# Kernel tuning notes

Hardware: AMD Instinct MI355X
Metric: run time of the kernel (lower is better)

The kernel has to match this reference:

```python
import jax, jax.numpy as jnp
import numpy as np

N_NODES = 50000
N_EDGES = 600000
IN_DIM = 128
OUT_DIM = 128
N_REL = 32
N_BASES = 4
BN_EPS = 1e-5


def setup_inputs() -> dict:
    key = jax.random.key(0)
    ks = jax.random.split(key, 8)
    entity_emb = jax.random.normal(ks[0], (N_NODES, IN_DIM), dtype=jnp.float32)
    bases = jax.random.normal(ks[1], (N_BASES, IN_DIM, OUT_DIM), dtype=jnp.float32) * 0.05
    coefficients = jax.random.normal(ks[2], (N_REL, N_BASES), dtype=jnp.float32) * 0.5
    W_loop = jax.random.normal(ks[3], (IN_DIM, OUT_DIM), dtype=jnp.float32) * 0.05
    b_loop = jnp.zeros((OUT_DIM,), dtype=jnp.float32)
    gamma = jnp.ones((OUT_DIM,), dtype=jnp.float32)
    beta = jnp.zeros((OUT_DIM,), dtype=jnp.float32)
    edge_index = jax.random.randint(ks[4], (2, N_EDGES), 0, N_NODES, dtype=jnp.int32)
    edge_type = jax.random.randint(ks[5], (N_EDGES,), 0, N_REL, dtype=jnp.int32)
    return {"entity_emb": entity_emb, "bases": bases, "coefficients": coefficients,
            "W_loop": W_loop, "b_loop": b_loop, "gamma": gamma, "beta": beta,
            "edge_index": edge_index, "edge_type": edge_type}


def reference(entity_emb, bases, coefficients, W_loop, b_loop, gamma, beta, edge_index, edge_type):
    N = entity_emb.shape[0]
    # self-loop linear
    out = entity_emb @ W_loop + b_loop  # [N, out_dim]
    # basis decomposition: per-relation weight W[r] = sum_b coeff[r,b] * bases[b]
    W = jnp.einsum('rb,bio->rio', coefficients, bases)  # [R, in, out]
    src, dst = edge_index[0], edge_index[1]
    # per-edge message: entity_emb[src_e] @ W[edge_type_e]  (vectorizes the per-relation loop)
    msg = jnp.einsum('ei,eio->eo', entity_emb[src], W[edge_type])  # [E, out]
    out = out + jax.ops.segment_sum(msg, dst, num_segments=N)
    # degree normalization (in-degree over all edges, clamped at 1)
    deg = jax.ops.segment_sum(jnp.ones_like(dst, dtype=out.dtype), dst, num_segments=N)
    out = out / jnp.maximum(deg, 1.0)[:, None]
    # BatchNorm1d (training mode: biased batch stats over node dim)
    mean = jnp.mean(out, axis=0)
    var = jnp.mean((out - mean) ** 2, axis=0)
    out = (out - mean) / jnp.sqrt(var + BN_EPS) * gamma + beta
    return jax.nn.relu(out)
```

## Files before the change

kernel.cpp:

```cpp
#include <hip/hip_runtime.h>
#include <cstdint>

#define NN 50000
#define NE 600000
#define NPAIRS 1563
#define GSTRIDE 512

typedef unsigned short ushort_t;
typedef __bf16 bf16_t;
typedef __attribute__((ext_vector_type(8))) bf16_t bf16x8;
typedef __attribute__((ext_vector_type(8))) ushort_t ushort8;
typedef __attribute__((ext_vector_type(4))) float f32x4;
typedef __attribute__((ext_vector_type(2))) float f32x2;

#define WT_OFF   0ul
#define XG_OFF   40960ul
#define XBF_OFF  16040960ul
#define CNT_OFF  19240960ul
#define CUR_OFF  19290960ul
#define BSUM_OFF 19340960ul
#define BSCN_OFF 19341088ul
#define CS_OFF   19341216ul
#define CSQ_OFF  19341344ul

__device__ __forceinline__ float2 bf2_to_f2(uint32_t u) {
    float2 r;
    r.x = __uint_as_float(u << 16);
    r.y = __uint_as_float(u & 0xffff0000u);
    return r;
}

__device__ __forceinline__ ushort_t f2bf(float f) {
    uint32_t u = __float_as_uint(f);
    u = (u + 0x7fffu + ((u >> 16) & 1u)) >> 16;
    return (ushort_t)u;
}

__device__ __forceinline__ uint32_t f2bf2(float x, float y) {
    return (uint32_t)f2bf(x) | ((uint32_t)f2bf(y) << 16);
}

__device__ __forceinline__ void async_copy16(const void* g, void* l) {
    __builtin_amdgcn_global_load_lds(
        (const __attribute__((address_space(1))) void*)g,
        (__attribute__((address_space(3))) void*)l, 16, 0, 0);
}

__global__ __launch_bounds__(256) void k_prep(
    const float* __restrict__ Wl, const float* __restrict__ bases,
    ushort_t* __restrict__ WT)
{
    const int i = blockIdx.x * 256 + threadIdx.x;
    if (i >= 128 * 640) return;
    const int n = i / 640;
    const int kk = i - n * 640;
    float v;
    if (kk < 128) v = Wl[kk * 128 + n];
    else {
        const int j = kk - 128;
        v = bases[(size_t)(j >> 7) * 16384 + (j & 127) * 128 + n];
    }
    WT[i] = f2bf(v);
}

__global__ __launch_bounds__(256) void k_cast(
    const float* __restrict__ X, ushort_t* __restrict__ Xbf,
    ushort_t* __restrict__ XG)
{
    __shared__ ushort_t L[16][136];
    const int tid = threadIdx.x;
    const int tile = blockIdx.x;
    {
        const int row = tid >> 4, gc = tid & 15;
        const int node = tile * 16 + row;
        const float4* p = (const float4*)(X + (size_t)node * 128 + gc * 8);
        const float4 a = p[0], b = p[1];
        ushort_t t8[8] = { f2bf(a.x), f2bf(a.y), f2bf(a.z), f2bf(a.w),
                           f2bf(b.x), f2bf(b.y), f2bf(b.z), f2bf(b.w) };
        const uint4 v = *(const uint4*)t8;
        *(uint4*)&L[row][gc * 8] = v;
        *(uint4*)(Xbf + (size_t)node * 128 + gc * 8) = v;
    }
    __syncthreads();
    {
        const int g = tid >> 4, r2 = tid & 15;
        const uint4 u = *(const uint4*)&L[r2][g * 8];
        *(uint4*)(XG + (size_t)tile * 10240 + g * 128 + r2 * 8) = u;
    }
}

__global__ __launch_bounds__(256) void k_hist(
    const int* __restrict__ eidx, int* __restrict__ cnt)
{
    const int* __restrict__ dst = eidx + NE;
    for (int e = blockIdx.x * 256 + threadIdx.x; e < NE; e += gridDim.x * 256)
        atomicAdd(cnt + dst[e], 1);
}

__global__ __launch_bounds__(256) void k_scan1(
    const int* __restrict__ cnt, int* __restrict__ curs, int* __restrict__ bsum)
{
    __shared__ int sh[256];
    const int tid = threadIdx.x;
    const int i0 = blockIdx.x * 512 + tid * 2;
    const int v0 = (i0 < NN) ? cnt[i0] : 0;
    const int v1 = (i0 + 1 < NN) ? cnt[i0 + 1] : 0;
    int s = v0 + v1;
    sh[tid] = s;
    __syncthreads();
#pragma unroll
    for (int off = 1; off < 256; off <<= 1) {
        int t = (tid >= off) ? sh[tid - off] : 0;
        __syncthreads();
        sh[tid] += t;
        __syncthreads();
    }
    const int excl = sh[tid] - s;
    if (i0 < NN) curs[i0] = excl;
    if (i0 + 1 < NN) curs[i0 + 1] = excl + v0;
    if (tid == 255) bsum[blockIdx.x] = sh[255];
}

__global__ __launch_bounds__(128) void k_scan2(
    const int* __restrict__ bsum, int* __restrict__ bscan, int nblk)
{
    __shared__ int sh[128];
    const int tid = threadIdx.x;
    int v = (tid < nblk) ? bsum[tid] : 0;
    sh[tid] = v;
    __syncthreads();
#pragma unroll
    for (int off = 1; off < 128; off <<= 1) {
        int t = (tid >= off) ? sh[tid - off] : 0;
        __syncthreads();
        sh[tid] += t;
        __syncthreads();
    }
    if (tid < nblk) bscan[tid] = sh[tid] - v;
}

__global__ __launch_bounds__(256) void k_scan3(
    int* __restrict__ curs, const int* __restrict__ bscan)
{
    const int add = bscan[blockIdx.x];
    const int i0 = blockIdx.x * 512 + threadIdx.x * 2;
    if (i0 < NN) curs[i0] += add;
    if (i0 + 1 < NN) curs[i0 + 1] += add;
}

__global__ __launch_bounds__(256) void k_scatter(
    const int* __restrict__ eidx, const int* __restrict__ etype,
    int* __restrict__ curs, uint32_t* __restrict__ epack)
{
    const int* __restrict__ src = eidx;
    const int* __restrict__ dst = eidx + NE;
    for (int e = blockIdx.x * 256 + threadIdx.x; e < NE; e += gridDim.x * 256) {
        const int d = dst[e];
        const int pos = atomicAdd(curs + d, 1);
        epack[pos] = (uint32_t)src[e] | ((uint32_t)etype[e] << 16);
    }
}

__device__ __forceinline__ void accum_pk(
    const uint4 xv, const float4 cw, f32x2* m2)
{
    f32x2 x2[4];
    float2 p;
    p = bf2_to_f2(xv.x); x2[0] = f32x2{p.x, p.y};
    p = bf2_to_f2(xv.y); x2[1] = f32x2{p.x, p.y};
    p = bf2_to_f2(xv.z); x2[2] = f32x2{p.x, p.y};
    p = bf2_to_f2(xv.w); x2[3] = f32x2{p.x, p.y};
#pragma unroll
    for (int c2 = 0; c2 < 4; ++c2) {
        m2[0 * 4 + c2] += cw.x * x2[c2];
        m2[1 * 4 + c2] += cw.y * x2[c2];
        m2[2 * 4 + c2] += cw.z * x2[c2];
        m2[3 * 4 + c2] += cw.w * x2[c2];
    }
}

__global__ __launch_bounds__(256, 4) void k_gather(
    const ushort_t* __restrict__ Xbf, const uint32_t* __restrict__ epack,
    const int* __restrict__ cnt, const int* __restrict__ curs,
    const float* __restrict__ coeff, ushort_t* __restrict__ XG)
{
    const int lane = threadIdx.x & 63;
    const int w = threadIdx.x >> 6;
    const int sub = lane >> 4;
    const int k = lane & 15;
    const int tile = blockIdx.x;
    const int d = tile * 16 + w * 4 + sub;

    const int n = cnt[d];
    const int end = curs[d];
    int j = end - n;

    f32x2 m2[16];
#pragma unroll
    for (int i = 0; i < 16; ++i) m2[i] = f32x2{0.f, 0.f};

    for (; j + 7 < end; j += 8) {
        uint32_t ep[8];
#pragma unroll
        for (int i = 0; i < 8; ++i) ep[i] = epack[j + i];
        uint4 xv[8];
        float4 cw[8];
#pragma unroll
        for (int i = 0; i < 8; ++i) {
            const int s = ep[i] & 0xffff;
            const int t = ep[i] >> 16;
            xv[i] = *(const uint4*)(Xbf + (size_t)s * 128 + k * 8);
            cw[i] = *(const float4*)(coeff + t * 4);
        }
#pragma unroll
        for (int i = 0; i < 8; ++i) accum_pk(xv[i], cw[i], m2);
    }
    if (j + 3 < end) {
        uint32_t ep[4];
#pragma unroll
        for (int i = 0; i < 4; ++i) ep[i] = epack[j + i];
        uint4 xv[4];
        float4 cw[4];
#pragma unroll
        for (int i = 0; i < 4; ++i) {
            const int s = ep[i] & 0xffff;
            const int t = ep[i] >> 16;
            xv[i] = *(const uint4*)(Xbf + (size_t)s * 128 + k * 8);
            cw[i] = *(const float4*)(coeff + t * 4);
        }
#pragma unroll
        for (int i = 0; i < 4; ++i) accum_pk(xv[i], cw[i], m2);
        j += 4;
    }
    for (; j < end; ++j) {
        const uint32_t ep = epack[j];
        const int s = ep & 0xffff;
        const int t = ep >> 16;
        const uint4 xv = *(const uint4*)(Xbf + (size_t)s * 128 + k * 8);
        const float4 cw = *(const float4*)(coeff + t * 4);
        accum_pk(xv, cw, m2);
    }

    uint32_t* gb = (uint32_t*)(XG + (size_t)tile * 10240);
#pragma unroll
    for (int b = 0; b < 4; ++b) {
        uint4 v;
        v.x = f2bf2(m2[b * 4 + 0][0], m2[b * 4 + 0][1]);
        v.y = f2bf2(m2[b * 4 + 1][0], m2[b * 4 + 1][1]);
        v.z = f2bf2(m2[b * 4 + 2][0], m2[b * 4 + 2][1]);
        v.w = f2bf2(m2[b * 4 + 3][0], m2[b * 4 + 3][1]);
        *(uint4*)(gb + (16 + b * 16 + k) * 64 + (w * 4 + sub) * 4) = v;
    }
}

__global__ __launch_bounds__(256, 1) void k_gemm_f(
    const ushort_t* __restrict__ XG, const ushort_t* __restrict__ WT,
    const float* __restrict__ bl, const int* __restrict__ cnt,
    float* __restrict__ out, float* __restrict__ colsum,
    float* __restrict__ colsq)
{
    __shared__ ushort_t As[2][2][10240];
    const int tid = threadIdx.x;
    const int lane = tid & 63;
    const int w = tid >> 6;
    const int m = lane & 15;
    const int quad = lane >> 4;

    auto stage = [&](ushort_t* __restrict__ d0, ushort_t* __restrict__ d1,
                     int pr) {
        const ushort_t* base = XG + (size_t)pr * 20480 +
                               (size_t)(w >> 1) * 10240;
        ushort_t* d = (w >> 1) ? d1 : d0;
        const int off0 = (w & 1) * 10;
#pragma unroll
        for (int j = 0; j < 10; ++j) {
            const int off = off0 + j;
            async_copy16(base + off * 512 + lane * 8, d + off * 512);
        }
    };

    const ushort_t* bp0 = WT + (size_t)(w * 32 + m) * 640 + quad * 8;
    const ushort_t* bp1 = bp0 + 16 * 640;
    ushort8 B0[20], B1[20];
    const float blv0 = bl[w * 32 + m];
    const float blv1 = bl[w * 32 + 16 + m];
    float s0 = 0.f, q0 = 0.f, s1 = 0.f, q1 = 0.f;

    auto compute = [&](const ushort_t* __restrict__ A0,
                       const ushort_t* __restrict__ A1, int pr) {
        f32x4 cc[2][2];
#pragma unroll
        for (int rt = 0; rt < 2; ++rt)
#pragma unroll
            for (int ct = 0; ct < 2; ++ct)
#pragma unroll
                for (int i = 0; i < 4; ++i) cc[rt][ct][i] = 0.f;

#pragma unroll
        for (int c = 0; c < 20; ++c) {
            const int aoff = (c * 4 + quad) * 128 + m * 8;
            const bf16x8 a0 = __builtin_bit_cast(bf16x8, *(const ushort8*)&A0[aoff]);
            const bf16x8 a1 = __builtin_bit_cast(bf16x8, *(const ushort8*)&A1[aoff]);
            const bf16x8 b0 = __builtin_bit_cast(bf16x8, B0[c]);
            const bf16x8 b1 = __builtin_bit_cast(bf16x8, B1[c]);
            cc[0][0] = __builtin_amdgcn_mfma_f32_16x16x32_bf16(a0, b0, cc[0][0], 0, 0, 0);
            cc[0][1] = __builtin_amdgcn_mfma_f32_16x16x32_bf16(a0, b1, cc[0][1], 0, 0, 0);
            cc[1][0] = __builtin_amdgcn_mfma_f32_16x16x32_bf16(a1, b0, cc[1][0], 0, 0, 0);
            cc[1][1] = __builtin_amdgcn_mfma_f32_16x16x32_bf16(a1, b1, cc[1][1], 0, 0, 0);
        }

        const int row0 = pr * 32;
#pragma unroll
        for (int rt = 0; rt < 2; ++rt) {
            const int rowb = row0 + rt * 16 + quad * 4;
#pragma unroll
            for (int r = 0; r < 4; ++r) {
                const int row = rowb + r;
                if (row < NN) {
                    const int dg = cnt[row];
                    const float inv = 1.0f / (float)((dg > 0) ? dg : 1);
                    float* po = out + (size_t)row * 128 + w * 32 + m;
                    const float v0 = (cc[rt][0][r] + blv0) * inv;
                    const float v1 = (cc[rt][1][r] + blv1) * inv;
                    po[0]  = v0;
                    po[16] = v1;
                    s0 += v0; q0 += v0 * v0;
                    s1 += v1; q1 += v1 * v1;
                }
            }
        }
    };

    int p = blockIdx.x;
    stage(As[0][0], As[0][1], p);
#pragma unroll
    for (int c = 0; c < 20; ++c) {
        B0[c] = *(const ushort8*)(bp0 + c * 32);
        B1[c] = *(const ushort8*)(bp1 + c * 32);
    }
    __syncthreads();

    while (true) {
        int pn = p + GSTRIDE;
        if (pn < NPAIRS) stage(As[1][0], As[1][1], pn);
        compute(As[0][0], As[0][1], p);
        if (pn >= NPAIRS) break;
        __syncthreads();
        p = pn;

        pn = p + GSTRIDE;
        if (pn < NPAIRS) stage(As[0][0], As[0][1], pn);
        compute(As[1][0], As[1][1], p);
        if (pn >= NPAIRS) break;
        __syncthreads();
        p = pn;
    }

    s0 += __shfl_down(s0, 32); q0 += __shfl_down(q0, 32);
    s0 += __shfl_down(s0, 16); q0 += __shfl_down(q0, 16);
    s1 += __shfl_down(s1, 32); q1 += __shfl_down(q1, 32);
    s1 += __shfl_down(s1, 16); q1 += __shfl_down(q1, 16);
    if (lane < 16) {
        atomicAdd(colsum + w * 32 + lane, s0);
        atomicAdd(colsq  + w * 32 + lane, q0);
        atomicAdd(colsum + w * 32 + 16 + lane, s1);
        atomicAdd(colsq  + w * 32 + 16 + lane, q1);
    }
}

__global__ __launch_bounds__(256) void k_bn_relu(
    float* __restrict__ out, const float* __restrict__ colsum,
    const float* __restrict__ colsq, const float* __restrict__ gamma,
    const float* __restrict__ beta)
{
    __shared__ float sc[128], sh[128];
    const int tid = threadIdx.x;
    if (tid < 128) {
        const float mean = colsum[tid] * (1.0f / NN);
        const float var = colsq[tid] * (1.0f / NN) - mean * mean;
        const float g = gamma[tid] * rsqrtf(var + 1e-5f);
        sc[tid] = g;
        sh[tid] = beta[tid] - mean * g;
    }
    __syncthreads();
    const int total = NN * 32;
    for (int i = blockIdx.x * 256 + tid; i < total; i += gridDim.x * 256) {
        const int c = (i & 31) << 2;
        float4 v = *(float4*)(out + (size_t)i * 4);
        v.x = fmaxf(fmaf(v.x, sc[c + 0], sh[c + 0]), 0.f);
        v.y = fmaxf(fmaf(v.y, sc[c + 1], sh[c + 1]), 0.f);
        v.z = fmaxf(fmaf(v.z, sc[c + 2], sh[c + 2]), 0.f);
        v.w = fmaxf(fmaf(v.w, sc[c + 3], sh[c + 3]), 0.f);
        *(float4*)(out + (size_t)i * 4) = v;
    }
}

extern "C" void kernel_launch(void* const* d_in, const int* in_sizes, int n_in,
                              void* d_out, int out_size, void* d_ws, size_t ws_size,
                              hipStream_t stream)
{
    const float* X      = (const float*)d_in[0];
    const float* bases  = (const float*)d_in[1];
    const float* coeff  = (const float*)d_in[2];
    const float* Wl     = (const float*)d_in[3];
    const float* bl     = (const float*)d_in[4];
    const float* gamma  = (const float*)d_in[5];
    const float* beta   = (const float*)d_in[6];
    const int*   eidx   = (const int*)d_in[7];
    const int*   etype  = (const int*)d_in[8];
    float* out = (float*)d_out;

    float* ws = (float*)d_ws;
    ushort_t* WT     = (ushort_t*)(ws + WT_OFF);
    ushort_t* XG     = (ushort_t*)(ws + XG_OFF);
    ushort_t* Xbf    = (ushort_t*)(ws + XBF_OFF);
    int*      cnt    = (int*)(ws + CNT_OFF);
    int*      curs   = (int*)(ws + CUR_OFF);
    int*      bsum   = (int*)(ws + BSUM_OFF);
    int*      bscan  = (int*)(ws + BSCN_OFF);
    float*    colsum = ws + CS_OFF;
    float*    colsq  = ws + CSQ_OFF;
    uint32_t* epack  = (uint32_t*)d_out;

    hipMemsetAsync(cnt, 0, (CSQ_OFF + 128 - CNT_OFF) * sizeof(float), stream);

    const int nblk_scan = (NN + 511) / 512;

    k_prep<<<(128 * 640 + 255) / 256, 256, 0, stream>>>(Wl, bases, WT);
    k_cast<<<3125, 256, 0, stream>>>(X, Xbf, XG);
    k_hist<<<2048, 256, 0, stream>>>(eidx, cnt);
    k_scan1<<<nblk_scan, 256, 0, stream>>>(cnt, curs, bsum);
    k_scan2<<<1, 128, 0, stream>>>(bsum, bscan, nblk_scan);
    k_scan3<<<nblk_scan, 256, 0, stream>>>(curs, bscan);
    k_scatter<<<2048, 256, 0, stream>>>(eidx, etype, curs, epack);
    k_gather<<<3125, 256, 0, stream>>>(Xbf, epack, cnt, curs, coeff, XG);
    k_gemm_f<<<GSTRIDE, 256, 0, stream>>>(XG, WT, bl, cnt, out, colsum, colsq);
    k_bn_relu<<<1024, 256, 0, stream>>>(out, colsum, colsq, gamma, beta);
}
```

Measured before the change: 251.9 us.

## Fuse prep/cast/hist kernels, read Xbf directly in GEMM, fold BN into GEMM via grid barrier

Merges the weight-prep, bf16 cast and degree-histogram kernels into one launch. The cast no longer writes the transposed X copy into the XG buffer; the GEMM now stages that self-loop slice straight from Xbf, so XG shrinks to only the gathered-basis part. The separate BatchNorm+ReLU kernel is replaced by a software grid barrier (atomic counter plus spin) at the end of the GEMM, after which each block normalizes its own rows. This saves launches and one pass of traffic, but relies on all 512 GEMM blocks being co-resident (launch bounds raised to 2 per CU) and uses scattered scalar accesses to the output in the epilogue.

```diff
diff --git a/kernel.cpp b/kernel.cpp
--- a/kernel.cpp
+++ b/kernel.cpp
@@ -14,14 +14,15 @@
 typedef __attribute__((ext_vector_type(2))) float f32x2;
 
 #define WT_OFF   0ul
-#define XG_OFF   40960ul
-#define XBF_OFF  16040960ul
-#define CNT_OFF  19240960ul
-#define CUR_OFF  19290960ul
-#define BSUM_OFF 19340960ul
-#define BSCN_OFF 19341088ul
-#define CS_OFF   19341216ul
-#define CSQ_OFF  19341344ul
+#define XGG_OFF  40960ul
+#define XBF_OFF  12845056ul
+#define CNT_OFF  16046080ul
+#define CUR_OFF  16096080ul
+#define BSUM_OFF 16146080ul
+#define BSCN_OFF 16146208ul
+#define CS_OFF   16146336ul
+#define CSQ_OFF  16146464ul
+#define DONE_OFF 16146592ul
 
 __device__ __forceinline__ float2 bf2_to_f2(uint32_t u) {
     float2 r;
@@ -46,55 +47,39 @@
         (__attribute__((address_space(3))) void*)l, 16, 0, 0);
 }
 
-__global__ __launch_bounds__(256) void k_prep(
-    const float* __restrict__ Wl, const float* __restrict__ bases,
-    ushort_t* __restrict__ WT)
-{
-    const int i = blockIdx.x * 256 + threadIdx.x;
-    if (i >= 128 * 640) return;
-    const int n = i / 640;
-    const int kk = i - n * 640;
-    float v;
-    if (kk < 128) v = Wl[kk * 128 + n];
-    else {
-        const int j = kk - 128;
-        v = bases[(size_t)(j >> 7) * 16384 + (j & 127) * 128 + n];
-    }
-    WT[i] = f2bf(v);
-}
-
-__global__ __launch_bounds__(256) void k_cast(
-    const float* __restrict__ X, ushort_t* __restrict__ Xbf,
-    ushort_t* __restrict__ XG)
-{
-    __shared__ ushort_t L[16][136];
+__global__ __launch_bounds__(256) void k_pre(
+    const float* __restrict__ X, const float* __restrict__ Wl,
+    const float* __restrict__ bases, const int* __restrict__ eidx,
+    ushort_t* __restrict__ WT, ushort_t* __restrict__ Xbf,
+    int* __restrict__ cnt)
+{
+    const int b = blockIdx.x;
     const int tid = threadIdx.x;
-    const int tile = blockIdx.x;
-    {
+    if (b < 320) {
+        const int i = b * 256 + tid;
+        const int n = i / 640;
+        const int kk = i - n * 640;
+        float v;
+        if (kk < 128) v = Wl[kk * 128 + n];
+        else {
+            const int j = kk - 128;
+            v = bases[(size_t)(j >> 7) * 16384 + (j & 127) * 128 + n];
+        }
+        WT[i] = f2bf(v);
+    } else if (b < 3445) {
+        const int tile = b - 320;
         const int row = tid >> 4, gc = tid & 15;
         const int node = tile * 16 + row;
         const float4* p = (const float4*)(X + (size_t)node * 128 + gc * 8);
-        const float4 a = p[0], b = p[1];
+        const float4 a = p[0], c = p[1];
         ushort_t t8[8] = { f2bf(a.x), f2bf(a.y), f2bf(a.z), f2bf(a.w),
-                           f2bf(b.x), f2bf(b.y), f2bf(b.z), f2bf(b.w) };
-        const uint4 v = *(const uint4*)t8;
-        *(uint4*)&L[row][gc * 8] = v;
-        *(uint4*)(Xbf + (size_t)node * 128 + gc * 8) = v;
-    }
-    __syncthreads();
-    {
-        const int g = tid >> 4, r2 = tid & 15;
-        const uint4 u = *(const uint4*)&L[r2][g * 8];
-        *(uint4*)(XG + (size_t)tile * 10240 + g * 128 + r2 * 8) = u;
-    }
-}
-
-__global__ __launch_bounds__(256) void k_hist(
-    const int* __restrict__ eidx, int* __restrict__ cnt)
-{
-    const int* __restrict__ dst = eidx + NE;
-    for (int e = blockIdx.x * 256 + threadIdx.x; e < NE; e += gridDim.x * 256)
-        atomicAdd(cnt + dst[e], 1);
+                           f2bf(c.x), f2bf(c.y), f2bf(c.z), f2bf(c.w) };
+        *(uint4*)(Xbf + (size_t)node * 128 + gc * 8) = *(const uint4*)t8;
+    } else {
+        const int* __restrict__ dst = eidx + NE;
+        for (int e = (b - 3445) * 256 + tid; e < NE; e += 2048 * 256)
+            atomicAdd(cnt + dst[e], 1);
+    }
 }
 
 __global__ __launch_bounds__(256) void k_scan1(
@@ -182,7 +167,7 @@
 __global__ __launch_bounds__(256, 4) void k_gather(
     const ushort_t* __restrict__ Xbf, const uint32_t* __restrict__ epack,
     const int* __restrict__ cnt, const int* __restrict__ curs,
-    const float* __restrict__ coeff, ushort_t* __restrict__ XG)
+    const float* __restrict__ coeff, ushort_t* __restrict__ XG_G)
 {
     const int lane = threadIdx.x & 63;
     const int w = threadIdx.x >> 6;
@@ -241,7 +226,7 @@
         accum_pk(xv, cw, m2);
     }
 
-    uint32_t* gb = (uint32_t*)(XG + (size_t)tile * 10240);
+    uint32_t* gb = (uint32_t*)(XG_G + (size_t)tile * 8192);
 #pragma unroll
     for (int b = 0; b < 4; ++b) {
         uint4 v;
@@ -249,15 +234,17 @@
         v.y = f2bf2(m2[b * 4 + 1][0], m2[b * 4 + 1][1]);
         v.z = f2bf2(m2[b * 4 + 2][0], m2[b * 4 + 2][1]);
         v.w = f2bf2(m2[b * 4 + 3][0], m2[b * 4 + 3][1]);
-        *(uint4*)(gb + (16 + b * 16 + k) * 64 + (w * 4 + sub) * 4) = v;
-    }
-}
-
-__global__ __launch_bounds__(256, 1) void k_gemm_f(
-    const ushort_t* __restrict__ XG, const ushort_t* __restrict__ WT,
-    const float* __restrict__ bl, const int* __restrict__ cnt,
-    float* __restrict__ out, float* __restrict__ colsum,
-    float* __restrict__ colsq)
+        *(uint4*)(gb + (b * 16 + k) * 64 + (w * 4 + sub) * 4) = v;
+    }
+}
+
+__global__ __launch_bounds__(256, 2) void k_gemm_f(
+    const ushort_t* __restrict__ XG_G, const ushort_t* __restrict__ WT,
+    const ushort_t* __restrict__ Xbf, const float* __restrict__ bl,
+    const int* __restrict__ cnt, const float* __restrict__ gamma,
+    const float* __restrict__ beta, float* __restrict__ out,
+    float* __restrict__ colsum, float* __restrict__ colsq,
+    int* __restrict__ done)
 {
     __shared__ ushort_t As[2][2][10240];
     const int tid = threadIdx.x;
@@ -268,14 +255,22 @@
 
     auto stage = [&](ushort_t* __restrict__ d0, ushort_t* __restrict__ d1,
                      int pr) {
-        const ushort_t* base = XG + (size_t)pr * 20480 +
-                               (size_t)(w >> 1) * 10240;
-        ushort_t* d = (w >> 1) ? d1 : d0;
+        const int tl = w >> 1;
+        const int tile = pr * 2 + tl;
+        ushort_t* d = tl ? d1 : d0;
         const int off0 = (w & 1) * 10;
 #pragma unroll
         for (int j = 0; j < 10; ++j) {
             const int off = off0 + j;
-            async_copy16(base + off * 512 + lane * 8, d + off * 512);
+            const ushort_t* src;
+            if (off < 4) {
+                const int node = tile * 16 + (lane & 15);
+                const int g = off * 4 + (lane >> 4);
+                src = Xbf + (size_t)node * 128 + g * 8;
+            } else {
+                src = XG_G + (size_t)tile * 8192 + (off - 4) * 512 + lane * 8;
+            }
+            async_copy16(src, d + off * 512);
         }
     };
 
@@ -366,32 +361,50 @@
         atomicAdd(colsum + w * 32 + 16 + lane, s1);
         atomicAdd(colsq  + w * 32 + 16 + lane, q1);
     }
-}
-
-__global__ __launch_bounds__(256) void k_bn_relu(
-    float* __restrict__ out, const float* __restrict__ colsum,
-    const float* __restrict__ colsq, const float* __restrict__ gamma,
-    const float* __restrict__ beta)
-{
-    __shared__ float sc[128], sh[128];
-    const int tid = threadIdx.x;
-    if (tid < 128) {
-        const float mean = colsum[tid] * (1.0f / NN);
-        const float var = colsq[tid] * (1.0f / NN) - mean * mean;
-        const float g = gamma[tid] * rsqrtf(var + 1e-5f);
-        sc[tid] = g;
-        sh[tid] = beta[tid] - mean * g;
-    }
+
     __syncthreads();
-    const int total = NN * 32;
-    for (int i = blockIdx.x * 256 + tid; i < total; i += gridDim.x * 256) {
-        const int c = (i & 31) << 2;
-        float4 v = *(float4*)(out + (size_t)i * 4);
-        v.x = fmaxf(fmaf(v.x, sc[c + 0], sh[c + 0]), 0.f);
-        v.y = fmaxf(fmaf(v.y, sc[c + 1], sh[c + 1]), 0.f);
-        v.z = fmaxf(fmaf(v.z, sc[c + 2], sh[c + 2]), 0.f);
-        v.w = fmaxf(fmaf(v.w, sc[c + 3], sh[c + 3]), 0.f);
-        *(float4*)(out + (size_t)i * 4) = v;
+    if (tid == 0) {
+        __threadfence();
+        atomicAdd(done, 1);
+        while (__hip_atomic_load(done, __ATOMIC_ACQUIRE,
+                                 __HIP_MEMORY_SCOPE_AGENT) < GSTRIDE)
+            __builtin_amdgcn_s_sleep(4);
+    }
+    __syncthreads();
+
+    const int c0 = w * 32 + m, c1 = c0 + 16;
+    const float cs0 = __hip_atomic_load(colsum + c0, __ATOMIC_RELAXED,
+                                        __HIP_MEMORY_SCOPE_AGENT);
+    const float cq0 = __hip_atomic_load(colsq + c0, __ATOMIC_RELAXED,
+                                        __HIP_MEMORY_SCOPE_AGENT);
+    const float cs1 = __hip_atomic_load(colsum + c1, __ATOMIC_RELAXED,
+                                        __HIP_MEMORY_SCOPE_AGENT);
+    const float cq1 = __hip_atomic_load(colsq + c1, __ATOMIC_RELAXED,
+                                        __HIP_MEMORY_SCOPE_AGENT);
+    const float mean0 = cs0 * (1.0f / NN);
+    const float var0  = cq0 * (1.0f / NN) - mean0 * mean0;
+    const float g0 = gamma[c0] * rsqrtf(var0 + 1e-5f);
+    const float h0 = beta[c0] - mean0 * g0;
+    const float mean1 = cs1 * (1.0f / NN);
+    const float var1  = cq1 * (1.0f / NN) - mean1 * mean1;
+    const float g1 = gamma[c1] * rsqrtf(var1 + 1e-5f);
+    const float h1 = beta[c1] - mean1 * g1;
+
+    for (int pp = blockIdx.x; pp < NPAIRS; pp += GSTRIDE) {
+        const int row0 = pp * 32;
+#pragma unroll
+        for (int rt = 0; rt < 2; ++rt) {
+            const int rowb = row0 + rt * 16 + quad * 4;
+#pragma unroll
+            for (int r = 0; r < 4; ++r) {
+                const int row = rowb + r;
+                if (row < NN) {
+                    float* po = out + (size_t)row * 128 + w * 32 + m;
+                    po[0]  = fmaxf(fmaf(po[0],  g0, h0), 0.f);
+                    po[16] = fmaxf(fmaf(po[16], g1, h1), 0.f);
+                }
+            }
+        }
     }
 }
 
@@ -412,7 +425,7 @@
 
     float* ws = (float*)d_ws;
     ushort_t* WT     = (ushort_t*)(ws + WT_OFF);
-    ushort_t* XG     = (ushort_t*)(ws + XG_OFF);
+    ushort_t* XG_G   = (ushort_t*)(ws + XGG_OFF);
     ushort_t* Xbf    = (ushort_t*)(ws + XBF_OFF);
     int*      cnt    = (int*)(ws + CNT_OFF);
     int*      curs   = (int*)(ws + CUR_OFF);
@@ -420,20 +433,19 @@
     int*      bscan  = (int*)(ws + BSCN_OFF);
     float*    colsum = ws + CS_OFF;
     float*    colsq  = ws + CSQ_OFF;
+    int*      done   = (int*)(ws + DONE_OFF);
     uint32_t* epack  = (uint32_t*)d_out;
 
-    hipMemsetAsync(cnt, 0, (CSQ_OFF + 128 - CNT_OFF) * sizeof(float), stream);
+    hipMemsetAsync(cnt, 0, (DONE_OFF + 1 - CNT_OFF) * sizeof(float), stream);
 
     const int nblk_scan = (NN + 511) / 512;
 
-    k_prep<<<(128 * 640 + 255) / 256, 256, 0, stream>>>(Wl, bases, WT);
-    k_cast<<<3125, 256, 0, stream>>>(X, Xbf, XG);
-    k_hist<<<2048, 256, 0, stream>>>(eidx, cnt);
+    k_pre<<<5493, 256, 0, stream>>>(X, Wl, bases, eidx, WT, Xbf, cnt);
     k_scan1<<<nblk_scan, 256, 0, stream>>>(cnt, curs, bsum);
     k_scan2<<<1, 128, 0, stream>>>(bsum, bscan, nblk_scan);
     k_scan3<<<nblk_scan, 256, 0, stream>>>(curs, bscan);
     k_scatter<<<2048, 256, 0, stream>>>(eidx, etype, curs, epack);
-    k_gather<<<3125, 256, 0, stream>>>(Xbf, epack, cnt, curs, coeff, XG);
-    k_gemm_f<<<GSTRIDE, 256, 0, stream>>>(XG, WT, bl, cnt, out, colsum, colsq);
-    k_bn_relu<<<1024, 256, 0, stream>>>(out, colsum, colsq, gamma, beta);
-}
+    k_gather<<<3125, 256, 0, stream>>>(Xbf, epack, cnt, curs, coeff, XG_G);
+    k_gemm_f<<<GSTRIDE, 256, 0, stream>>>(XG_G, WT, Xbf, bl, cnt,
+                                          gamma, beta, out, colsum, colsq, done);
+}
```

Result: slower. 300.4 us (+19.3%).
